# Kernel tuning notes

Hardware: AMD Instinct MI355X
Metric: run time of the kernel (lower is better)

Reference implementation:

```python
import jax, jax.numpy as jnp
import numpy as np

B, L, K = 16, 8192, 128


def setup_inputs() -> dict:
    key = jax.random.key(0)
    k1, k2, k3 = jax.random.split(key, 3)
    # tracer positions in [-pi, pi]
    x0 = (jax.random.uniform(k1, (B, L), dtype=jnp.float32) * 2.0 - 1.0) * jnp.pi
    y0 = (jax.random.uniform(k2, (B, L), dtype=jnp.float32) * 2.0 - 1.0) * jnp.pi
    psi = jax.random.normal(k3, (B, K, K), dtype=jnp.float32)
    return {"x0": x0, "y0": y0, "psi": psi}


def reference(x0, y0, psi):
    # x0, y0: (B, L) float32; psi: (B, K, K) float32
    Kdim = psi.shape[-1]
    # wavenumbers, fftshifted, matching torch.fft.fftshift(torch.fft.fftfreq(K, d=1/K))
    kx = jnp.fft.fftshift(jnp.fft.fftfreq(Kdim, d=1.0 / Kdim)).astype(jnp.float32)
    ky = kx  # identical construction
    # fftshifted 2D spectrum: psi_hat[b, i, j] pairs with phase x*kx[j] + y*ky[i]
    # (torch meshgrid indexing='xy': KX[i,j]=kx[j], KY[i,j]=ky[i])
    psi_hat = jnp.fft.fftshift(jnp.fft.fft2(psi), axes=(-2, -1)).astype(jnp.complex64)
    # separable phase: exp(i(x*kx_j + y*ky_i)) = Ex[b,l,j] * Ey[b,l,i]
    Ex = jnp.exp(1j * (x0[..., None] * kx)).astype(jnp.complex64)  # (B, L, K)
    Ey = jnp.exp(1j * (y0[..., None] * ky)).astype(jnp.complex64)  # (B, L, K)
    # contract j first: (B, L, K) intermediate instead of (B, L, K*K)
    tmp = jnp.einsum('bij,blj->bli', psi_hat, Ex)
    psi_x = jnp.real(jnp.einsum('bli,bli->bl', tmp, Ey)) / (Kdim ** 2)
    return psi_x.astype(jnp.float32)
```

## Files before the change

kernel.cpp:

```cpp
#include <hip/hip_runtime.h>
#include <math.h>

#ifndef M_PI
#define M_PI 3.14159265358979323846
#endif

typedef _Float16 half8v __attribute__((ext_vector_type(8)));
typedef _Float16 half2v __attribute__((ext_vector_type(2)));
typedef float float4v __attribute__((ext_vector_type(4)));

constexpr int KDIM = 128;
constexpr int LTOT = 8192;
constexpr int TILE_L = 64;
constexpr int NT = 256;
constexpr int WSTR = 136;

__global__ __launch_bounds__(NT, 4) void main_kernel(const float* __restrict__ x0,
        const float* __restrict__ y0, const float* __restrict__ psi,
        float* __restrict__ out) {
    __shared__ _Float16 wxT[TILE_L][WSTR];
    __shared__ _Float16 wyT[TILE_L][WSTR];
    __shared__ float ndh[KDIM], ndl[KDIM], ndh2[KDIM], ndl2[KDIM];
    __shared__ float s64A[2][TILE_L];
    __shared__ float partial[4][TILE_L];
    __shared__ float cbred[4];

    const int tid = threadIdx.x;
    const int lane = tid & 63;
    const int w = tid >> 6;
    const int bid = blockIdx.x;
    const int b = bid >> 7;
    const int l0 = (bid & 127) * TILE_L;
    const int qd = lane >> 4;
    const int ln = lane & 15;

    const float* Pb = psi + (size_t)b * 16384;

    if (tid < KDIM) {
        double d = (double)tid * (M_PI / 64.0);
        float h = (float)d;
        ndh[tid] = h; ndl[tid] = (float)(d - (double)h);
        double d2 = d - 2.0 * M_PI;
        float h2 = (float)d2;
        ndh2[tid] = h2; ndl2[tid] = (float)(d2 - (double)h2);
    }

    const int col = tid & 127;
    const int mat = col >> 6;
    const int l = col & 63;
    const int hf = tid >> 7;
    const float* src = mat ? y0 : x0;
    const float pos = src[(size_t)b * LTOT + l0 + l];
    const float s64 = sinf(64.0f * pos);
    float sa, ca;
    sincosf(0.5f * pos, &sa, &ca);
    float cs_s, cs_c;
    if (hf == 0) { cs_s = sa; cs_c = ca; s64A[mat][l] = s64; }
    else         { cs_s = -ca; cs_c = sa; }
    __syncthreads();

    _Float16* dst = mat ? &wyT[l][0] : &wxT[l][0];
    const float CB  = 0.9996988186962042f,  SB  = 0.024541228522912288f;
    const float C16 = 0.9238795325112867f,  S16 = 0.3826834323650898f;
    const float step = (float)(M_PI / 64.0);
#pragma unroll
    for (int kk = 0; kk < 4; ++kk) {
        float ws_ = cs_s, wc_ = cs_c;
        const int q0 = 64 * hf + 16 * kk;
#pragma unroll
        for (int h8 = 0; h8 < 2; ++h8) {
            _Float16 buf[8];
#pragma unroll
            for (int j = 0; j < 8; ++j) {
                const int q = q0 + 8 * h8 + j;
                const float num = (j & 1) ? -s64 : s64;
                float wv;
                if (__builtin_expect(fabsf(ws_) >= 2e-3f, 1)) {
                    wv = num * wc_ * __builtin_amdgcn_rcpf(ws_);
                } else {
                    float ta = pos - step * (float)q;
                    float nh, nl;
                    if (ta > -1.0f) { nh = ndh[q];  nl = ndl[q]; }
                    else            { nh = ndh2[q]; nl = ndl2[q]; }
                    float u = (pos - nh) - nl;
                    if (fabsf(u) < 1e-7f) {
                        wv = 128.0f;
                    } else {
                        float hh = 0.5f * u;
                        float s2 = hh * (1.0f - 0.16666667f * hh * hh);
                        float c2 = 1.0f - 0.5f * hh * hh;
                        wv = num * c2 * __builtin_amdgcn_rcpf(s2);
                    }
                }
                buf[j] = (_Float16)wv;
                float ns = ws_ * CB - wc_ * SB;
                wc_ = wc_ * CB + ws_ * SB;
                ws_ = ns;
            }
            *(half8v*)&dst[q0 + 8 * h8] = *(half8v*)buf;
        }
        float ns = cs_s * C16 - cs_c * S16;
        cs_c = cs_c * C16 + cs_s * S16;
        cs_s = ns;
    }
    __syncthreads();

    float4v a_raw[2][2];
#pragma unroll
    for (int mi = 0; mi < 2; ++mi) {
        const float* rp = Pb + (32 * w + 16 * mi + ln) * 128 + 8 * qd;
        a_raw[mi][0] = *(const float4v*)(rp);
        a_raw[mi][1] = *(const float4v*)(rp + 4);
    }

    float4v acc[2][4];
#pragma unroll
    for (int mi = 0; mi < 2; ++mi)
#pragma unroll
        for (int ni = 0; ni < 4; ++ni) acc[mi][ni] = (float4v){0.f, 0.f, 0.f, 0.f};

    float cbs = 0.0f;
#pragma unroll
    for (int k = 0; k < 4; ++k) {
        half8v af[2];
#pragma unroll
        for (int mi = 0; mi < 2; ++mi) {
#pragma unroll
            for (int j = 0; j < 4; ++j) {
                af[mi][j]     = (_Float16)a_raw[mi][0][j];
                af[mi][4 + j] = (_Float16)a_raw[mi][1][j];
            }
            cbs += (a_raw[mi][0].x - a_raw[mi][0].y) + (a_raw[mi][0].z - a_raw[mi][0].w)
                 + (a_raw[mi][1].x - a_raw[mi][1].y) + (a_raw[mi][1].z - a_raw[mi][1].w);
        }
        if (k < 3) {
#pragma unroll
            for (int mi = 0; mi < 2; ++mi) {
                const float* rp = Pb + (32 * w + 16 * mi + ln) * 128 + (k + 1) * 32 + 8 * qd;
                a_raw[mi][0] = *(const float4v*)(rp);
                a_raw[mi][1] = *(const float4v*)(rp + 4);
            }
        }
#pragma unroll
        for (int ni = 0; ni < 4; ++ni) {
            half8v bf = *(const half8v*)&wxT[16 * ni + ln][k * 32 + 8 * qd];
#pragma unroll
            for (int mi = 0; mi < 2; ++mi)
                acc[mi][ni] = __builtin_amdgcn_mfma_f32_16x16x32_f16(af[mi], bf, acc[mi][ni], 0, 0, 0);
        }
    }

    if (ln & 1) cbs = -cbs;
#pragma unroll
    for (int off = 1; off < 64; off <<= 1) cbs += __shfl_xor(cbs, off, 64);
    if (lane == 0) cbred[w] = cbs;

    float part[4];
#pragma unroll
    for (int ni = 0; ni < 4; ++ni) {
        float s = 0.f;
#pragma unroll
        for (int mi = 0; mi < 2; ++mi) {
            const _Float16* wp = &wyT[16 * ni + ln][32 * w + 16 * mi + 4 * qd];
            half2v w01 = *(const half2v*)(wp);
            half2v w23 = *(const half2v*)(wp + 2);
            s += acc[mi][ni][0] * (float)w01[0] + acc[mi][ni][1] * (float)w01[1]
               + acc[mi][ni][2] * (float)w23[0] + acc[mi][ni][3] * (float)w23[1];
        }
        s += __shfl_xor(s, 16, 64);
        s += __shfl_xor(s, 32, 64);
        part[ni] = s;
    }
    if (qd == 0) {
#pragma unroll
        for (int ni = 0; ni < 4; ++ni) partial[w][16 * ni + ln] = part[ni];
    }
    __syncthreads();

    if (tid < TILE_L) {
        float cb = (cbred[0] + cbred[1]) + (cbred[2] + cbred[3]);
        float s = (partial[0][tid] + partial[1][tid]) + (partial[2][tid] + partial[3][tid]);
        s -= s64A[0][tid] * s64A[1][tid] * cb;
        out[(size_t)b * LTOT + l0 + tid] = s * (1.0f / 16384.0f);
    }
}

extern "C" void kernel_launch(void* const* d_in, const int* in_sizes, int n_in,
                              void* d_out, int out_size, void* d_ws, size_t ws_size,
                              hipStream_t stream) {
    const float* x0  = (const float*)d_in[0];
    const float* y0  = (const float*)d_in[1];
    const float* psi = (const float*)d_in[2];
    float* out = (float*)d_out;
    (void)d_ws; (void)ws_size;

    main_kernel<<<16 * (LTOT / TILE_L), NT, 0, stream>>>(x0, y0, psi, out);
}
```

Before: 82.93 us.

## Compute y-weights in registers during epilogue instead of staging through LDS

Drops the shared-memory wyT table. Each lane now recomputes its y-direction Dirichlet-kernel weights directly in the epilogue from the y position, using per-lane rotation offsets and applying them straight to the MFMA accumulators. The aim is to cut LDS footprint and the store/load round trip so that more blocks fit per CU, and launch bounds are raised to 7 to match. The cost is extra sincos and reciprocal work in the epilogue, and only 128 threads now build the x table, so the prologue has less parallelism.

```diff
diff --git a/kernel.cpp b/kernel.cpp
--- a/kernel.cpp
+++ b/kernel.cpp
@@ -6,7 +6,6 @@
 #endif
 
 typedef _Float16 half8v __attribute__((ext_vector_type(8)));
-typedef _Float16 half2v __attribute__((ext_vector_type(2)));
 typedef float float4v __attribute__((ext_vector_type(4)));
 
 constexpr int KDIM = 128;
@@ -15,13 +14,14 @@
 constexpr int NT = 256;
 constexpr int WSTR = 136;
 
-__global__ __launch_bounds__(NT, 4) void main_kernel(const float* __restrict__ x0,
+__global__ __launch_bounds__(NT, 7) void main_kernel(const float* __restrict__ x0,
         const float* __restrict__ y0, const float* __restrict__ psi,
         float* __restrict__ out) {
     __shared__ _Float16 wxT[TILE_L][WSTR];
-    __shared__ _Float16 wyT[TILE_L][WSTR];
     __shared__ float ndh[KDIM], ndl[KDIM], ndh2[KDIM], ndl2[KDIM];
-    __shared__ float s64A[2][TILE_L];
+    __shared__ float s64X[TILE_L];
+    __shared__ float posyL[TILE_L];
+    __shared__ float s64Y[TILE_L];
     __shared__ float partial[4][TILE_L];
     __shared__ float cbred[4];
 
@@ -45,44 +45,160 @@
         ndh2[tid] = h2; ndl2[tid] = (float)(d2 - (double)h2);
     }
 
-    const int col = tid & 127;
-    const int mat = col >> 6;
-    const int l = col & 63;
-    const int hf = tid >> 7;
-    const float* src = mat ? y0 : x0;
-    const float pos = src[(size_t)b * LTOT + l0 + l];
-    const float s64 = sinf(64.0f * pos);
-    float sa, ca;
-    sincosf(0.5f * pos, &sa, &ca);
-    float cs_s, cs_c;
-    if (hf == 0) { cs_s = sa; cs_c = ca; s64A[mat][l] = s64; }
-    else         { cs_s = -ca; cs_c = sa; }
+    const int l = tid & 63;
+    const int hf = (tid >> 6) & 1;
+    float pos = 0.f, s64 = 0.f, cs_s = 0.f, cs_c = 0.f;
+    if (tid < 128) {
+        pos = x0[(size_t)b * LTOT + l0 + l];
+        s64 = sinf(64.0f * pos);
+        float sa, ca;
+        sincosf(0.5f * pos, &sa, &ca);
+        if (hf == 0) { cs_s = sa; cs_c = ca; s64X[l] = s64; }
+        else         { cs_s = -ca; cs_c = sa; }
+    } else if (tid < 192) {
+        const int i = tid - 128;
+        float py = y0[(size_t)b * LTOT + l0 + i];
+        posyL[i] = py;
+        s64Y[i] = sinf(64.0f * py);
+    }
     __syncthreads();
 
-    _Float16* dst = mat ? &wyT[l][0] : &wxT[l][0];
     const float CB  = 0.9996988186962042f,  SB  = 0.024541228522912288f;
     const float C16 = 0.9238795325112867f,  S16 = 0.3826834323650898f;
     const float step = (float)(M_PI / 64.0);
-#pragma unroll
-    for (int kk = 0; kk < 4; ++kk) {
-        float ws_ = cs_s, wc_ = cs_c;
-        const int q0 = 64 * hf + 16 * kk;
-#pragma unroll
-        for (int h8 = 0; h8 < 2; ++h8) {
-            _Float16 buf[8];
-#pragma unroll
-            for (int j = 0; j < 8; ++j) {
-                const int q = q0 + 8 * h8 + j;
-                const float num = (j & 1) ? -s64 : s64;
+    if (tid < 128) {
+        _Float16* dst = &wxT[l][0];
+#pragma unroll
+        for (int kk = 0; kk < 4; ++kk) {
+            float ws_ = cs_s, wc_ = cs_c;
+            const int q0 = 64 * hf + 16 * kk;
+#pragma unroll
+            for (int h8 = 0; h8 < 2; ++h8) {
+                _Float16 buf[8];
+#pragma unroll
+                for (int j = 0; j < 8; ++j) {
+                    const int q = q0 + 8 * h8 + j;
+                    const float num = (j & 1) ? -s64 : s64;
+                    float wv;
+                    if (__builtin_expect(fabsf(ws_) >= 2e-3f, 1)) {
+                        wv = num * wc_ * __builtin_amdgcn_rcpf(ws_);
+                    } else {
+                        float ta = pos - step * (float)q;
+                        float nh, nl;
+                        if (ta > -1.0f) { nh = ndh[q];  nl = ndl[q]; }
+                        else            { nh = ndh2[q]; nl = ndl2[q]; }
+                        float u = (pos - nh) - nl;
+                        if (fabsf(u) < 1e-7f) {
+                            wv = 128.0f;
+                        } else {
+                            float hh = 0.5f * u;
+                            float s2 = hh * (1.0f - 0.16666667f * hh * hh);
+                            float c2 = 1.0f - 0.5f * hh * hh;
+                            wv = num * c2 * __builtin_amdgcn_rcpf(s2);
+                        }
+                    }
+                    buf[j] = (_Float16)wv;
+                    float ns = ws_ * CB - wc_ * SB;
+                    wc_ = wc_ * CB + ws_ * SB;
+                    ws_ = ns;
+                }
+                *(half8v*)&dst[q0 + 8 * h8] = *(half8v*)buf;
+            }
+            float ns = cs_s * C16 - cs_c * S16;
+            cs_c = cs_c * C16 + cs_s * S16;
+            cs_s = ns;
+        }
+    }
+    __syncthreads();
+
+    float4v a_raw[2][2];
+#pragma unroll
+    for (int mi = 0; mi < 2; ++mi) {
+        const float* rp = Pb + (32 * w + 16 * mi + ln) * 128 + 8 * qd;
+        a_raw[mi][0] = *(const float4v*)(rp);
+        a_raw[mi][1] = *(const float4v*)(rp + 4);
+    }
+
+    float4v acc[2][4];
+#pragma unroll
+    for (int mi = 0; mi < 2; ++mi)
+#pragma unroll
+        for (int ni = 0; ni < 4; ++ni) acc[mi][ni] = (float4v){0.f, 0.f, 0.f, 0.f};
+
+    float cbs = 0.0f;
+#pragma unroll
+    for (int k = 0; k < 4; ++k) {
+        half8v af[2];
+#pragma unroll
+        for (int mi = 0; mi < 2; ++mi) {
+#pragma unroll
+            for (int j = 0; j < 4; ++j) {
+                af[mi][j]     = (_Float16)a_raw[mi][0][j];
+                af[mi][4 + j] = (_Float16)a_raw[mi][1][j];
+            }
+            cbs += (a_raw[mi][0].x - a_raw[mi][0].y) + (a_raw[mi][0].z - a_raw[mi][0].w)
+                 + (a_raw[mi][1].x - a_raw[mi][1].y) + (a_raw[mi][1].z - a_raw[mi][1].w);
+        }
+        if (k < 3) {
+#pragma unroll
+            for (int mi = 0; mi < 2; ++mi) {
+                const float* rp = Pb + (32 * w + 16 * mi + ln) * 128 + (k + 1) * 32 + 8 * qd;
+                a_raw[mi][0] = *(const float4v*)(rp);
+                a_raw[mi][1] = *(const float4v*)(rp + 4);
+            }
+        }
+#pragma unroll
+        for (int ni = 0; ni < 4; ++ni) {
+            half8v bf = *(const half8v*)&wxT[16 * ni + ln][k * 32 + 8 * qd];
+#pragma unroll
+            for (int mi = 0; mi < 2; ++mi)
+                acc[mi][ni] = __builtin_amdgcn_mfma_f32_16x16x32_f16(af[mi], bf, acc[mi][ni], 0, 0, 0);
+        }
+    }
+
+    if (ln & 1) cbs = -cbs;
+#pragma unroll
+    for (int off = 1; off < 64; off <<= 1) cbs += __shfl_xor(cbs, off, 64);
+    if (lane == 0) cbred[w] = cbs;
+
+    const float R2 = 0.7071067811865476f;
+    const float CQ = (qd == 0) ? 1.0f : (qd == 1) ? 0.9951847266721969f
+                   : (qd == 2) ? 0.9807852804032304f : 0.9569403357322088f;
+    const float SQ = (qd == 0) ? 0.0f : (qd == 1) ? 0.0980171403295606f
+                   : (qd == 2) ? 0.19509032201612825f : 0.29028467725446233f;
+    const float CW = (w == 0) ? 1.0f : (w == 1) ? R2 : (w == 2) ? 0.0f : -R2;
+    const float SW = (w == 0) ? 0.0f : (w == 1) ? R2 : (w == 2) ? 1.0f : R2;
+
+    float part[4];
+#pragma unroll
+    for (int ni = 0; ni < 4; ++ni) {
+        const int ly = 16 * ni + ln;
+        const float py = posyL[ly];
+        const float n0 = s64Y[ly];
+        float sy, cy;
+        sincosf(0.5f * py, &sy, &cy);
+        float s1 = sy * CQ - cy * SQ;
+        float c1 = cy * CQ + sy * SQ;
+        float s0 = s1 * CW - c1 * SW;
+        float c0 = c1 * CW + s1 * SW;
+        float ssum = 0.f;
+#pragma unroll
+        for (int mi = 0; mi < 2; ++mi) {
+            float ws_ = s0, wc_ = c0;
+            const int pbase = 32 * w + 16 * mi + 4 * qd;
+#pragma unroll
+            for (int reg = 0; reg < 4; ++reg) {
+                const int p = pbase + reg;
+                const float num = (reg & 1) ? -n0 : n0;
                 float wv;
                 if (__builtin_expect(fabsf(ws_) >= 2e-3f, 1)) {
                     wv = num * wc_ * __builtin_amdgcn_rcpf(ws_);
                 } else {
-                    float ta = pos - step * (float)q;
+                    float ta = py - step * (float)p;
                     float nh, nl;
-                    if (ta > -1.0f) { nh = ndh[q];  nl = ndl[q]; }
-                    else            { nh = ndh2[q]; nl = ndl2[q]; }
-                    float u = (pos - nh) - nl;
+                    if (ta > -1.0f) { nh = ndh[p];  nl = ndl[p]; }
+                    else            { nh = ndh2[p]; nl = ndl2[p]; }
+                    float u = (py - nh) - nl;
                     if (fabsf(u) < 1e-7f) {
                         wv = 128.0f;
                     } else {
@@ -92,84 +208,20 @@
                         wv = num * c2 * __builtin_amdgcn_rcpf(s2);
                     }
                 }
-                buf[j] = (_Float16)wv;
+                ssum += acc[mi][ni][reg] * wv;
                 float ns = ws_ * CB - wc_ * SB;
                 wc_ = wc_ * CB + ws_ * SB;
                 ws_ = ns;
             }
-            *(half8v*)&dst[q0 + 8 * h8] = *(half8v*)buf;
-        }
-        float ns = cs_s * C16 - cs_c * S16;
-        cs_c = cs_c * C16 + cs_s * S16;
-        cs_s = ns;
-    }
-    __syncthreads();
-
-    float4v a_raw[2][2];
-#pragma unroll
-    for (int mi = 0; mi < 2; ++mi) {
-        const float* rp = Pb + (32 * w + 16 * mi + ln) * 128 + 8 * qd;
-        a_raw[mi][0] = *(const float4v*)(rp);
-        a_raw[mi][1] = *(const float4v*)(rp + 4);
-    }
-
-    float4v acc[2][4];
-#pragma unroll
-    for (int mi = 0; mi < 2; ++mi)
-#pragma unroll
-        for (int ni = 0; ni < 4; ++ni) acc[mi][ni] = (float4v){0.f, 0.f, 0.f, 0.f};
-
-    float cbs = 0.0f;
-#pragma unroll
-    for (int k = 0; k < 4; ++k) {
-        half8v af[2];
-#pragma unroll
-        for (int mi = 0; mi < 2; ++mi) {
-#pragma unroll
-            for (int j = 0; j < 4; ++j) {
-                af[mi][j]     = (_Float16)a_raw[mi][0][j];
-                af[mi][4 + j] = (_Float16)a_raw[mi][1][j];
-            }
-            cbs += (a_raw[mi][0].x - a_raw[mi][0].y) + (a_raw[mi][0].z - a_raw[mi][0].w)
-                 + (a_raw[mi][1].x - a_raw[mi][1].y) + (a_raw[mi][1].z - a_raw[mi][1].w);
-        }
-        if (k < 3) {
-#pragma unroll
-            for (int mi = 0; mi < 2; ++mi) {
-                const float* rp = Pb + (32 * w + 16 * mi + ln) * 128 + (k + 1) * 32 + 8 * qd;
-                a_raw[mi][0] = *(const float4v*)(rp);
-                a_raw[mi][1] = *(const float4v*)(rp + 4);
-            }
-        }
-#pragma unroll
-        for (int ni = 0; ni < 4; ++ni) {
-            half8v bf = *(const half8v*)&wxT[16 * ni + ln][k * 32 + 8 * qd];
-#pragma unroll
-            for (int mi = 0; mi < 2; ++mi)
-                acc[mi][ni] = __builtin_amdgcn_mfma_f32_16x16x32_f16(af[mi], bf, acc[mi][ni], 0, 0, 0);
-        }
-    }
-
-    if (ln & 1) cbs = -cbs;
-#pragma unroll
-    for (int off = 1; off < 64; off <<= 1) cbs += __shfl_xor(cbs, off, 64);
-    if (lane == 0) cbred[w] = cbs;
-
-    float part[4];
-#pragma unroll
-    for (int ni = 0; ni < 4; ++ni) {
-        float s = 0.f;
-#pragma unroll
-        for (int mi = 0; mi < 2; ++mi) {
-            const _Float16* wp = &wyT[16 * ni + ln][32 * w + 16 * mi + 4 * qd];
-            half2v w01 = *(const half2v*)(wp);
-            half2v w23 = *(const half2v*)(wp + 2);
-            s += acc[mi][ni][0] * (float)w01[0] + acc[mi][ni][1] * (float)w01[1]
-               + acc[mi][ni][2] * (float)w23[0] + acc[mi][ni][3] * (float)w23[1];
-        }
-        s += __shfl_xor(s, 16, 64);
-        s += __shfl_xor(s, 32, 64);
-        part[ni] = s;
+            if (mi == 0) {
+                float ns = s0 * C16 - c0 * S16;
+                c0 = c0 * C16 + s0 * S16;
+                s0 = ns;
+            }
+        }
+        ssum += __shfl_xor(ssum, 16, 64);
+        ssum += __shfl_xor(ssum, 32, 64);
+        part[ni] = ssum;
     }
     if (qd == 0) {
 #pragma unroll
@@ -180,7 +232,7 @@
     if (tid < TILE_L) {
         float cb = (cbred[0] + cbred[1]) + (cbred[2] + cbred[3]);
         float s = (partial[0][tid] + partial[1][tid]) + (partial[2][tid] + partial[3][tid]);
-        s -= s64A[0][tid] * s64A[1][tid] * cb;
+        s -= s64X[tid] * s64Y[tid] * cb;
         out[(size_t)b * LTOT + l0 + tid] = s * (1.0f / 16384.0f);
     }
 }
```

Result: slower. 90.60 us (+9.2%).
